# Kernel optimization log

Hardware: AMD Instinct MI355X
Metric: run time of the kernel (lower is better)

The kernel has to match this reference:

```python
import jax, jax.numpy as jnp
import numpy as np

N, IN, OUT, T = 500000, 128, 64, 8

def setup_inputs() -> dict:
    key = jax.random.key(0)
    k1, k2, k3, k4 = jax.random.split(key, 4)
    x = jax.random.normal(k1, (N, IN), dtype=jnp.float32)
    node_type = jax.random.randint(k2, (N,), 0, T, dtype=jnp.int32)
    # per-type Linear weights, stored as [T, IN, OUT] so x @ W[t] matches torch Linear
    W = jax.random.normal(k3, (T, IN, OUT), dtype=jnp.float32) * (1.0 / np.sqrt(IN))
    b = jax.random.normal(k4, (T, OUT), dtype=jnp.float32) * 0.01
    return {"x": x, "node_type": node_type, "W": W, "b": b}

def reference(x, node_type, W, b):
    # emb_x[mask_t] = x[mask_t] @ W[t] + b[t], for each node type t.
    # Vectorized: loop over the small fixed number of types, masked accumulate.
    T_ = W.shape[0]
    out = jnp.zeros((x.shape[0], W.shape[2]), dtype=x.dtype)
    for t in range(T_):
        y_t = x @ W[t] + b[t]                      # [N, OUT]
        mask = (node_type == t)[:, None]           # [N, 1]
        out = jnp.where(mask, y_t, out)
    return out
```

## Files before the change

### kernel.cpp

```cpp
#include <hip/hip_runtime.h>
#include <hip/hip_bf16.h>

#define NT   8
#define INF  128
#define OUTF 64
#define BR   256

typedef __attribute__((ext_vector_type(8))) short short8;
typedef __attribute__((ext_vector_type(4))) float f32x4;

__device__ __forceinline__ short f2bf(float f) {
  __hip_bfloat16 h = __float2bfloat16(f);
  return __builtin_bit_cast(short, h);
}

__global__ void hl_wconv(const float* __restrict__ W, short* __restrict__ wbf) {
  const int tid   = blockIdx.x * blockDim.x + threadIdx.x;
  const int combo = tid >> 6;
  const int lane  = tid & 63;
  const int t = combo >> 4, s = (combo >> 2) & 3, nb = combo & 3;
  const int q = lane >> 4, c = lane & 15;
  const float* Wt = W + t * INF * OUTF;
  short8 v;
  #pragma unroll
  for (int j = 0; j < 8; ++j)
    v[j] = f2bf(Wt[(s * 32 + q * 8 + j) * OUTF + nb * 16 + c]);
  *(short8*)(wbf + (size_t)tid * 8) = v;
}

__global__ __launch_bounds__(256, 4) void hl_nb(
    const float* __restrict__ x, const int* __restrict__ nty,
    const short* __restrict__ wbf, const float* __restrict__ b,
    float* __restrict__ out, int N) {
  __shared__ int lcnt[NT], cbase[NT];
  __shared__ short lorder[BR];
  __shared__ int descs[NT + BR / 16];
  __shared__ int ndesc;

  const int tid   = threadIdx.x;
  const int base  = blockIdx.x * BR;
  const int nrows = min(BR, N - base);

  int myty = 0;
  if (tid < nrows) myty = nty[base + tid];
  if (tid < NT) lcnt[tid] = 0;
  __syncthreads();
  int myrank = 0;
  if (tid < nrows) myrank = atomicAdd(&lcnt[myty], 1);
  __syncthreads();
  if (tid < NT) {
    int o = 0;
    #pragma unroll
    for (int t = 0; t < NT; ++t) o += (t < tid) ? lcnt[t] : 0;
    cbase[tid] = o;
  }
  if (tid == 0) {
    int nd = 0, o = 0;
    for (int t = 0; t < NT; ++t) {
      const int cn = lcnt[t];
      for (int j = 0; j < cn; j += 16)
        descs[nd++] = t | (min(16, cn - j) << 3) | ((o + j) << 8);
      o += cn;
    }
    ndesc = nd;
  }
  __syncthreads();
  if (tid < nrows) lorder[cbase[myty] + myrank] = (short)tid;
  __syncthreads();

  const int wave = tid >> 6, lane = tid & 63;
  const int q = lane >> 4, c = lane & 15;
  const int nd = ndesc;
  const short* wp = wbf + lane * 8;

  for (int i = wave; i < nd; i += 4) {
    const int d = descs[i];
    const int t = d & 7, valid = (d >> 3) & 31, loff = d >> 8;

    const int am   = c < valid ? c : valid - 1;
    const int lrow = lorder[loff + am];
    const float* xr = x + (size_t)(base + lrow) * INF;
    short8 A[4];
    #pragma unroll
    for (int s = 0; s < 4; ++s) {
      f32x4 v0 = *(const f32x4*)(xr + s * 32 + q * 8);
      f32x4 v1 = *(const f32x4*)(xr + s * 32 + q * 8 + 4);
      short8 a;
      #pragma unroll
      for (int j = 0; j < 4; ++j) { a[j] = f2bf(v0[j]); a[j + 4] = f2bf(v1[j]); }
      A[s] = a;
    }

    f32x4 acc[4];
    #pragma unroll
    for (int nb = 0; nb < 4; ++nb) acc[nb] = (f32x4){0, 0, 0, 0};

    #pragma unroll
    for (int s = 0; s < 4; ++s) {
      #pragma unroll
      for (int nb = 0; nb < 4; ++nb) {
        short8 B = *(const short8*)(wp + (size_t)((t * 4 + s) * 4 + nb) * 512);
        acc[nb] = __builtin_amdgcn_mfma_f32_16x16x32_bf16(A[s], B, acc[nb], 0, 0, 0);
      }
    }

    float bv[4];
    #pragma unroll
    for (int nb = 0; nb < 4; ++nb) bv[nb] = b[t * OUTF + nb * 16 + c];
    #pragma unroll
    for (int r = 0; r < 4; ++r) {
      const int m = q * 4 + r;
      if (m < valid) {
        const int grow = base + lorder[loff + m];
        float* orow = out + (size_t)grow * OUTF + c;
        #pragma unroll
        for (int nb = 0; nb < 4; ++nb)
          orow[nb * 16] = acc[nb][r] + bv[nb];
      }
    }
  }
}

extern "C" void kernel_launch(void* const* d_in, const int* in_sizes, int n_in,
                              void* d_out, int out_size, void* d_ws, size_t ws_size,
                              hipStream_t stream) {
  const float* x  = (const float*)d_in[0];
  const int*   nt = (const int*)d_in[1];
  const float* W  = (const float*)d_in[2];
  const float* b  = (const float*)d_in[3];
  float* out = (float*)d_out;
  const int N = in_sizes[1];
  short* wbf = (short*)d_ws;

  hl_wconv<<<32, 256, 0, stream>>>(W, wbf);
  const int gb = (N + BR - 1) / BR;
  hl_nb<<<gb, 256, 0, stream>>>(x, nt, wbf, b, out, N);
}
```

Measured before the change: 424.6 us.

## Stage block's x tile into swizzled LDS as bf16 with coalesced loads

Each block now loads its 128 rows of x with fully coalesced float4 loads, converts them to bf16, and stores them in a swizzled shared-memory tile. The loads are split into two batches that overlap with the type-counting and ordering steps. The MFMA loop then reads A fragments from LDS instead of gathering scattered rows from global memory, and all B fragments are hoisted before the MFMAs. The block size is halved to 128 rows to fit the 32KB tile, which means more blocks and higher register and LDS pressure that may limit occupancy.

```diff
diff --git a/kernel.cpp b/kernel.cpp
--- a/kernel.cpp
+++ b/kernel.cpp
@@ -4,9 +4,10 @@
 #define NT   8
 #define INF  128
 #define OUTF 64
-#define BR   256
+#define BR   128
 
 typedef __attribute__((ext_vector_type(8))) short short8;
+typedef __attribute__((ext_vector_type(4))) short short4v;
 typedef __attribute__((ext_vector_type(4))) float f32x4;
 
 __device__ __forceinline__ short f2bf(float f) {
@@ -28,11 +29,12 @@
   *(short8*)(wbf + (size_t)tid * 8) = v;
 }
 
-__global__ __launch_bounds__(256, 4) void hl_nb(
+__global__ __launch_bounds__(256, 4) void hl_sb(
     const float* __restrict__ x, const int* __restrict__ nty,
     const short* __restrict__ wbf, const float* __restrict__ b,
     float* __restrict__ out, int N) {
-  __shared__ int lcnt[NT], cbase[NT];
+  __shared__ short xs[BR * 128];
+  __shared__ int lcnt[NT];
   __shared__ short lorder[BR];
   __shared__ int descs[NT + BR / 16];
   __shared__ int ndesc;
@@ -41,18 +43,47 @@
   const int base  = blockIdx.x * BR;
   const int nrows = min(BR, N - base);
 
+  if (tid < NT) lcnt[tid] = 0;
   int myty = 0;
   if (tid < nrows) myty = nty[base + tid];
-  if (tid < NT) lcnt[tid] = 0;
+
+  f32x4 va[8];
+  #pragma unroll
+  for (int k = 0; k < 8; ++k) {
+    const int f4 = tid + k * 256;
+    int row = f4 >> 5;
+    if (row >= nrows) row = nrows - 1;
+    va[k] = *(const f32x4*)(x + (size_t)(base + row) * INF + (f4 & 31) * 4);
+  }
   __syncthreads();
   int myrank = 0;
   if (tid < nrows) myrank = atomicAdd(&lcnt[myty], 1);
+
+  #pragma unroll
+  for (int k = 0; k < 8; ++k) {
+    const int f4 = tid + k * 256;
+    const int row = f4 >> 5, q4 = f4 & 31;
+    short4v s4;
+    s4[0] = f2bf(va[k][0]); s4[1] = f2bf(va[k][1]);
+    s4[2] = f2bf(va[k][2]); s4[3] = f2bf(va[k][3]);
+    *(short4v*)((char*)xs + row * 256 + ((q4 * 8) ^ ((row & 7) << 4))) = s4;
+  }
+
+  f32x4 vb[8];
+  #pragma unroll
+  for (int k = 0; k < 8; ++k) {
+    const int f4 = tid + (k + 8) * 256;
+    int row = f4 >> 5;
+    if (row >= nrows) row = nrows - 1;
+    vb[k] = *(const f32x4*)(x + (size_t)(base + row) * INF + (f4 & 31) * 4);
+  }
   __syncthreads();
-  if (tid < NT) {
-    int o = 0;
+
+  if (tid < nrows) {
+    int mycb = 0;
     #pragma unroll
-    for (int t = 0; t < NT; ++t) o += (t < tid) ? lcnt[t] : 0;
-    cbase[tid] = o;
+    for (int t = 0; t < NT; ++t) mycb += (t < myty) ? lcnt[t] : 0;
+    lorder[mycb + myrank] = (short)tid;
   }
   if (tid == 0) {
     int nd = 0, o = 0;
@@ -64,8 +95,16 @@
     }
     ndesc = nd;
   }
-  __syncthreads();
-  if (tid < nrows) lorder[cbase[myty] + myrank] = (short)tid;
+
+  #pragma unroll
+  for (int k = 0; k < 8; ++k) {
+    const int f4 = tid + (k + 8) * 256;
+    const int row = f4 >> 5, q4 = f4 & 31;
+    short4v s4;
+    s4[0] = f2bf(vb[k][0]); s4[1] = f2bf(vb[k][1]);
+    s4[2] = f2bf(vb[k][2]); s4[3] = f2bf(vb[k][3]);
+    *(short4v*)((char*)xs + row * 256 + ((q4 * 8) ^ ((row & 7) << 4))) = s4;
+  }
   __syncthreads();
 
   const int wave = tid >> 6, lane = tid & 63;
@@ -77,32 +116,31 @@
     const int d = descs[i];
     const int t = d & 7, valid = (d >> 3) & 31, loff = d >> 8;
 
+    short8 B[4][4];
+    #pragma unroll
+    for (int s = 0; s < 4; ++s)
+      #pragma unroll
+      for (int nb = 0; nb < 4; ++nb)
+        B[s][nb] = *(const short8*)(wp + (size_t)((t * 4 + s) * 4 + nb) * 512);
+
     const int am   = c < valid ? c : valid - 1;
     const int lrow = lorder[loff + am];
-    const float* xr = x + (size_t)(base + lrow) * INF;
+    const char* arow = (const char*)xs + lrow * 256;
+    const int sw = (lrow & 7) << 4;
     short8 A[4];
     #pragma unroll
-    for (int s = 0; s < 4; ++s) {
-      f32x4 v0 = *(const f32x4*)(xr + s * 32 + q * 8);
-      f32x4 v1 = *(const f32x4*)(xr + s * 32 + q * 8 + 4);
-      short8 a;
-      #pragma unroll
-      for (int j = 0; j < 4; ++j) { a[j] = f2bf(v0[j]); a[j + 4] = f2bf(v1[j]); }
-      A[s] = a;
-    }
+    for (int s = 0; s < 4; ++s)
+      A[s] = *(const short8*)(arow + ((s * 64 + q * 16) ^ sw));
 
     f32x4 acc[4];
     #pragma unroll
     for (int nb = 0; nb < 4; ++nb) acc[nb] = (f32x4){0, 0, 0, 0};
 
     #pragma unroll
-    for (int s = 0; s < 4; ++s) {
+    for (int s = 0; s < 4; ++s)
       #pragma unroll
-      for (int nb = 0; nb < 4; ++nb) {
-        short8 B = *(const short8*)(wp + (size_t)((t * 4 + s) * 4 + nb) * 512);
-        acc[nb] = __builtin_amdgcn_mfma_f32_16x16x32_bf16(A[s], B, acc[nb], 0, 0, 0);
-      }
-    }
+      for (int nb = 0; nb < 4; ++nb)
+        acc[nb] = __builtin_amdgcn_mfma_f32_16x16x32_bf16(A[s], B[s][nb], acc[nb], 0, 0, 0);
 
     float bv[4];
     #pragma unroll
@@ -134,5 +172,5 @@
 
   hl_wconv<<<32, 256, 0, stream>>>(W, wbf);
   const int gb = (N + BR - 1) / BR;
-  hl_nb<<<gb, 256, 0, stream>>>(x, nt, wbf, b, out, N);
+  hl_sb<<<gb, 256, 0, stream>>>(x, nt, wbf, b, out, N);
 }
```

Measured after the change: 393.4 us. 7.3% less time.

## Make node-type GEMM kernel persistent with double-buffered LDS staging of x

Applied to the files above, without the earlier changes.

Replaces the one-block-per-256-rows kernel with a persistent grid of up to 256 blocks of 512 threads. Each block loops over 128-row chunks and prefetches the next chunk's x rows into a second LDS buffer with asynchronous global-to-LDS loads, using an XOR swizzle to avoid bank conflicts. The next chunk's type bucketing runs while the current chunk's MFMAs execute. The aim is to hide global-load latency behind compute in this bandwidth-bound kernel. The cost is about 128KB of LDS per block, which limits each CU to one block, plus extra synchronisation and reliance on the async loads completing before the barrier.

```diff
diff --git a/kernel.cpp b/kernel.cpp
--- a/kernel.cpp
+++ b/kernel.cpp
@@ -4,7 +4,7 @@
 #define NT   8
 #define INF  128
 #define OUTF 64
-#define BR   256
+#define BR   128
 
 typedef __attribute__((ext_vector_type(8))) short short8;
 typedef __attribute__((ext_vector_type(4))) float f32x4;
@@ -28,96 +28,164 @@
   *(short8*)(wbf + (size_t)tid * 8) = v;
 }
 
-__global__ __launch_bounds__(256, 4) void hl_nb(
+__global__ __launch_bounds__(512, 2) void hl_pp(
     const float* __restrict__ x, const int* __restrict__ nty,
     const short* __restrict__ wbf, const float* __restrict__ b,
     float* __restrict__ out, int N) {
-  __shared__ int lcnt[NT], cbase[NT];
-  __shared__ short lorder[BR];
-  __shared__ int descs[NT + BR / 16];
-  __shared__ int ndesc;
-
-  const int tid   = threadIdx.x;
-  const int base  = blockIdx.x * BR;
-  const int nrows = min(BR, N - base);
-
-  int myty = 0;
-  if (tid < nrows) myty = nty[base + tid];
-  if (tid < NT) lcnt[tid] = 0;
+  __shared__ float xs[2][BR * INF];
+  __shared__ int   lcnt[2][NT];
+  __shared__ short lorder[2][BR];
+  __shared__ int   descs[2][16];
+  __shared__ int   ndesc[2];
+
+  const int tid  = threadIdx.x;
+  const int wave = tid >> 6, lane = tid & 63;
+  const int q = lane >> 4, c = lane & 15;
+  const int nchunks = (N + BR - 1) / BR;
+  const int ck0 = blockIdx.x;
+  const short* wp = wbf + lane * 8;
+  if (ck0 >= nchunks) return;
+
+  auto STAGE = [&](int ck, int bb) {
+    const int base = ck * BR;
+    const int nr = min(BR, N - base);
+    #pragma unroll
+    for (int j = 0; j < 8; ++j) {
+      const int pr = (wave * 8 + j) * 2;
+      const int r  = pr + (lane >> 5);
+      const int rc = (r < nr) ? r : (nr - 1);
+      const int sb = ((lane & 31) * 16) ^ ((r & 15) << 4);
+      const char* src = (const char*)(x + (size_t)(base + rc) * INF) + sb;
+      __builtin_amdgcn_global_load_lds(
+          (const __attribute__((address_space(1))) void*)src,
+          (__attribute__((address_space(3))) void*)(&xs[bb][0] + (size_t)(wave * 8 + j) * 256),
+          16, 0, 0);
+    }
+  };
+
+  if (tid < 2 * NT) ((int*)lcnt)[tid] = 0;
+  STAGE(ck0, 0);
+  const int base0 = ck0 * BR;
+  const int nr0 = min(BR, N - base0);
+  int ty0 = 0;
+  if (tid < nr0) ty0 = nty[base0 + tid];
   __syncthreads();
-  int myrank = 0;
-  if (tid < nrows) myrank = atomicAdd(&lcnt[myty], 1);
+  int rk0 = 0;
+  if (tid < nr0) rk0 = atomicAdd(&lcnt[0][ty0], 1);
   __syncthreads();
-  if (tid < NT) {
-    int o = 0;
+  if (tid < nr0) {
+    int cb = 0;
     #pragma unroll
-    for (int t = 0; t < NT; ++t) o += (t < tid) ? lcnt[t] : 0;
-    cbase[tid] = o;
+    for (int t = 0; t < NT; ++t) cb += (t < ty0) ? lcnt[0][t] : 0;
+    lorder[0][cb + rk0] = (short)tid;
   }
   if (tid == 0) {
-    int nd = 0, o = 0;
+    int nd = 0, o2 = 0;
     for (int t = 0; t < NT; ++t) {
-      const int cn = lcnt[t];
-      for (int j = 0; j < cn; j += 16)
-        descs[nd++] = t | (min(16, cn - j) << 3) | ((o + j) << 8);
-      o += cn;
-    }
-    ndesc = nd;
+      const int cn = lcnt[0][t];
+      for (int j2 = 0; j2 < cn; j2 += 16)
+        descs[0][nd++] = t | (min(16, cn - j2) << 3) | ((o2 + j2) << 8);
+      o2 += cn;
+    }
+    ndesc[0] = nd;
   }
   __syncthreads();
-  if (tid < nrows) lorder[cbase[myty] + myrank] = (short)tid;
-  __syncthreads();
-
-  const int wave = tid >> 6, lane = tid & 63;
-  const int q = lane >> 4, c = lane & 15;
-  const int nd = ndesc;
-  const short* wp = wbf + lane * 8;
-
-  for (int i = wave; i < nd; i += 4) {
-    const int d = descs[i];
-    const int t = d & 7, valid = (d >> 3) & 31, loff = d >> 8;
-
-    const int am   = c < valid ? c : valid - 1;
-    const int lrow = lorder[loff + am];
-    const float* xr = x + (size_t)(base + lrow) * INF;
-    short8 A[4];
-    #pragma unroll
-    for (int s = 0; s < 4; ++s) {
-      f32x4 v0 = *(const f32x4*)(xr + s * 32 + q * 8);
-      f32x4 v1 = *(const f32x4*)(xr + s * 32 + q * 8 + 4);
-      short8 a;
-      #pragma unroll
-      for (int j = 0; j < 4; ++j) { a[j] = f2bf(v0[j]); a[j + 4] = f2bf(v1[j]); }
-      A[s] = a;
-    }
-
-    f32x4 acc[4];
-    #pragma unroll
-    for (int nb = 0; nb < 4; ++nb) acc[nb] = (f32x4){0, 0, 0, 0};
-
-    #pragma unroll
-    for (int s = 0; s < 4; ++s) {
-      #pragma unroll
-      for (int nb = 0; nb < 4; ++nb) {
-        short8 B = *(const short8*)(wp + (size_t)((t * 4 + s) * 4 + nb) * 512);
-        acc[nb] = __builtin_amdgcn_mfma_f32_16x16x32_bf16(A[s], B, acc[nb], 0, 0, 0);
-      }
-    }
-
-    float bv[4];
-    #pragma unroll
-    for (int nb = 0; nb < 4; ++nb) bv[nb] = b[t * OUTF + nb * 16 + c];
-    #pragma unroll
-    for (int r = 0; r < 4; ++r) {
-      const int m = q * 4 + r;
-      if (m < valid) {
-        const int grow = base + lorder[loff + m];
-        float* orow = out + (size_t)grow * OUTF + c;
+
+  int cur = 0;
+  for (int ck = ck0; ck < nchunks; ck += gridDim.x, cur ^= 1) {
+    const int nxt = ck + gridDim.x;
+    const int o = cur ^ 1;
+    const bool hasnxt = (nxt < nchunks);
+
+    int tyn = 0, rkn = 0, nrn = 0;
+    if (hasnxt) {
+      STAGE(nxt, o);
+      const int bn = nxt * BR;
+      nrn = min(BR, N - bn);
+      if (tid < nrn) {
+        tyn = nty[bn + tid];
+        rkn = atomicAdd(&lcnt[o][tyn], 1);
+      }
+    }
+
+    const int base = ck * BR;
+    const int nd = ndesc[cur];
+    for (int i = wave; i < nd; i += 8) {
+      const int d = descs[cur][i];
+      const int t = d & 7, valid = (d >> 3) & 31, loff = d >> 8;
+
+      short8 B[4][4];
+      #pragma unroll
+      for (int s = 0; s < 4; ++s)
         #pragma unroll
         for (int nb = 0; nb < 4; ++nb)
-          orow[nb * 16] = acc[nb][r] + bv[nb];
-      }
-    }
+          B[s][nb] = *(const short8*)(wp + (size_t)((t * 4 + s) * 4 + nb) * 512);
+
+      const int am = c < valid ? c : valid - 1;
+      const int lr = lorder[cur][loff + am];
+      const char* xrow = (const char*)&xs[cur][lr * INF];
+      const int sw = (lr & 15) << 4;
+
+      f32x4 av[8];
+      #pragma unroll
+      for (int s = 0; s < 4; ++s) {
+        av[s * 2]     = *(const f32x4*)(xrow + ((s * 128 + q * 32) ^ sw));
+        av[s * 2 + 1] = *(const f32x4*)(xrow + ((s * 128 + q * 32 + 16) ^ sw));
+      }
+
+      f32x4 acc[4];
+      #pragma unroll
+      for (int nb = 0; nb < 4; ++nb) acc[nb] = (f32x4){0, 0, 0, 0};
+      #pragma unroll
+      for (int s = 0; s < 4; ++s) {
+        short8 a;
+        #pragma unroll
+        for (int j2 = 0; j2 < 4; ++j2) {
+          a[j2]     = f2bf(av[s * 2][j2]);
+          a[j2 + 4] = f2bf(av[s * 2 + 1][j2]);
+        }
+        #pragma unroll
+        for (int nb = 0; nb < 4; ++nb)
+          acc[nb] = __builtin_amdgcn_mfma_f32_16x16x32_bf16(a, B[s][nb], acc[nb], 0, 0, 0);
+      }
+
+      float bv[4];
+      #pragma unroll
+      for (int nb = 0; nb < 4; ++nb) bv[nb] = b[t * OUTF + nb * 16 + c];
+      #pragma unroll
+      for (int r = 0; r < 4; ++r) {
+        const int m = q * 4 + r;
+        if (m < valid) {
+          const int grow = base + lorder[cur][loff + m];
+          float* orow = out + (size_t)grow * OUTF + c;
+          #pragma unroll
+          for (int nb = 0; nb < 4; ++nb)
+            orow[nb * 16] = acc[nb][r] + bv[nb];
+        }
+      }
+    }
+
+    __syncthreads();
+    if (hasnxt) {
+      if (tid < nrn) {
+        int cb = 0;
+        #pragma unroll
+        for (int t = 0; t < NT; ++t) cb += (t < tyn) ? lcnt[o][t] : 0;
+        lorder[o][cb + rkn] = (short)tid;
+      }
+      if (tid == 0) {
+        int nd2 = 0, o2 = 0;
+        for (int t = 0; t < NT; ++t) {
+          const int cn = lcnt[o][t];
+          for (int j2 = 0; j2 < cn; j2 += 16)
+            descs[o][nd2++] = t | (min(16, cn - j2) << 3) | ((o2 + j2) << 8);
+          o2 += cn;
+        }
+        ndesc[o] = nd2;
+      }
+    }
+    if (tid < NT) lcnt[cur][tid] = 0;
+    __syncthreads();
   }
 }
 
@@ -133,6 +201,7 @@
   short* wbf = (short*)d_ws;
 
   hl_wconv<<<32, 256, 0, stream>>>(W, wbf);
-  const int gb = (N + BR - 1) / BR;
-  hl_nb<<<gb, 256, 0, stream>>>(x, nt, wbf, b, out, N);
-}
+  const int nchunks = (N + BR - 1) / BR;
+  const int gb = nchunks < 256 ? nchunks : 256;
+  hl_pp<<<gb, 512, 0, stream>>>(x, nt, wbf, b, out, N);
+}
```

Result: no change. 421.1 us (-0.8%).
